# Optimization experiments

Hardware: AMD Instinct MI355X
Metric: run time of the kernel (lower is better)

Reference implementation:

```python
import jax, jax.numpy as jnp
import numpy as np

B, SEQ, DIM = 2, 2048, 1024
H = 16
DH = DIM // H            # 64, head dim; LayerNorm is over this axis
LAT = 512
CTX = SEQ - LAT          # 1536
SCALE = DH ** -0.5
LN_EPS = 1e-5


def _rotary_cos_sin(n):
    # lucidrains RotaryEmbedding: inv_freq = 1/10000^(2i/d); emb = cat(freqs, freqs)
    inv_freq = 1.0 / (10000.0 ** (jnp.arange(0, DH, 2, dtype=jnp.float32) / DH))
    freqs = jnp.arange(n, dtype=jnp.float32)[:, None] * inv_freq[None, :]
    emb = jnp.concatenate([freqs, freqs], axis=-1)  # [n, DH]
    return jnp.cos(emb), jnp.sin(emb)


def _rotate_half(t):
    t1, t2 = jnp.split(t, 2, axis=-1)
    return jnp.concatenate([-t2, t1], axis=-1)


def _layernorm(t, g, b):
    m = jnp.mean(t, axis=-1, keepdims=True)
    v = jnp.var(t, axis=-1, keepdims=True)
    return (t - m) / jnp.sqrt(v + LN_EPS) * g + b


def setup_inputs() -> dict:
    key = jax.random.key(0)
    ks = jax.random.split(key, 4)
    x = jax.random.normal(ks[0], (B, SEQ, DIM), dtype=jnp.float32)
    Wq = jax.random.normal(ks[1], (DIM, DIM), dtype=jnp.float32) * 0.02
    Wkv = jax.random.normal(ks[2], (DIM, DIM), dtype=jnp.float32) * 0.02
    Wo = jax.random.normal(ks[3], (DIM, DIM), dtype=jnp.float32) * 0.02
    bo = jnp.zeros((DIM,), dtype=jnp.float32)
    ln_g = jnp.ones((DH,), dtype=jnp.float32)
    ln_b = jnp.zeros((DH,), dtype=jnp.float32)
    return {"x": x, "Wq": Wq, "Wkv": Wkv, "Wo": Wo, "bo": bo, "ln_g": ln_g, "ln_b": ln_b}


def reference(x, Wq, Wkv, Wo, bo, ln_g, ln_b):
    b, n, d = x.shape
    neg = -jnp.finfo(x.dtype).max

    # projections (torch Linear: y = x @ W.T)
    q = x @ Wq.T
    kv = x @ Wkv.T

    def split_heads(t):  # b n (h d) -> (b h) n d
        return t.reshape(b, n, H, DH).transpose(0, 2, 1, 3).reshape(b * H, n, DH)

    q = split_heads(q)
    kv = split_heads(kv)

    cos, sin = _rotary_cos_sin(n)  # [n, DH], broadcasts over (b h)
    q = q * cos + _rotate_half(q) * sin
    kv = kv * cos + _rotate_half(kv) * sin

    q_lat = q[:, CTX:] * SCALE   # [(bh), LAT, DH]
    q_ctx = q[:, :CTX] * SCALE   # [(bh), CTX, DH]

    lkv = _layernorm(kv, ln_g, ln_b)       # key layernorm over head dim
    lkv_ctx = lkv[:, :CTX]                 # per-position LN => slice equals norm(kv_ctx)

    # latent branch: latent queries over full sequence, causal only on latent block
    lsim = jnp.einsum('bid,bjd->bij', q_lat, lkv)  # [(bh), LAT, n]
    lat = n - CTX
    causal = jnp.triu(jnp.ones((lat, lat), dtype=bool), 1)
    mask = jnp.concatenate([jnp.zeros((lat, CTX), dtype=bool), causal], axis=-1)
    lsim = jnp.where(mask, neg, lsim)
    attn = jax.nn.softmax(lsim, axis=-1)
    out = jnp.einsum('bij,bjd->bid', attn, lkv)    # [(bh), LAT, DH]

    # context branch: context queries over context keys, NO causal mask
    lsim_ctx = jnp.einsum('bid,bjd->bij', q_ctx, lkv_ctx)
    attn_ctx = jax.nn.softmax(lsim_ctx, axis=-1)
    out_ctx = jnp.einsum('bij,bjd->bid', attn_ctx, lkv_ctx)  # [(bh), CTX, DH]

    def merge_heads(t):  # (b h) m d -> b m (h d)
        m = t.shape[1]
        return t.reshape(b, H, m, DH).transpose(0, 2, 1, 3).reshape(b, m, H * DH)

    # original concatenates latent output FIRST, then context
    out_all = jnp.concatenate([merge_heads(out), merge_heads(out_ctx)], axis=1)
    return out_all @ Wo.T + bo
```

## Files before the change

### kernel.cpp

```cpp
#include <hip/hip_runtime.h>
#include <cstdint>
#include <cstddef>

typedef unsigned short u16;
typedef __bf16 bf16x8 __attribute__((ext_vector_type(8)));
typedef __bf16 bf16x2 __attribute__((ext_vector_type(2)));
typedef float f32x4 __attribute__((ext_vector_type(4)));
typedef float f32x16 __attribute__((ext_vector_type(16)));

#define DEV __device__ __forceinline__

DEV float bf2f(u16 v) { union { unsigned u; float f; } x; x.u = ((unsigned)v) << 16; return x.f; }
DEV u16 f2bf(float f) {
  union { float f; unsigned u; } x; x.f = f;
  unsigned u = x.u + 0x7fffu + ((x.u >> 16) & 1u);
  return (u16)(u >> 16);
}

DEV float fexp2(float x) {
#if __has_builtin(__builtin_amdgcn_exp2f)
  return __builtin_amdgcn_exp2f(x);
#else
  return exp2f(x);
#endif
}

DEV f32x4 mfma16(bf16x8 a, bf16x8 b, f32x4 c) {
  return __builtin_amdgcn_mfma_f32_16x16x32_bf16(a, b, c, 0, 0, 0);
}
DEV f32x16 mfma32(bf16x8 a, bf16x8 b, f32x16 c) {
  return __builtin_amdgcn_mfma_f32_32x32x16_bf16(a, b, c, 0, 0, 0);
}

DEV void stage16(const void* g, void* l) {
#if __has_builtin(__builtin_amdgcn_global_load_lds)
  __builtin_amdgcn_global_load_lds((__attribute__((address_space(1))) void*)g,
                                   (__attribute__((address_space(3))) void*)l, 16, 0, 0);
#else
  *(uint4*)l = *(const uint4*)g;
#endif
}

DEV unsigned pkbf(float a, float b) {
  bf16x2 v = {(__bf16)a, (__bf16)b};
  return __builtin_bit_cast(unsigned, v);
}

DEV void plswap(unsigned& a, unsigned& b) {
#if __has_builtin(__builtin_amdgcn_permlane32_swap)
  auto r = __builtin_amdgcn_permlane32_swap(a, b, false, false);
  a = (unsigned)r[0];
  b = (unsigned)r[1];
#else
  unsigned sa = __shfl_xor((int)a, 32), sb = __shfl_xor((int)b, 32);
  bool hi = ((threadIdx.x & 63) >> 5) != 0;
  unsigned na = hi ? sb : a;
  unsigned nb = hi ? b : sa;
  a = na; b = nb;
#endif
}

__global__ __launch_bounds__(256) void cvt_all(const float* __restrict__ x,
                                               const float* __restrict__ Wq,
                                               const float* __restrict__ Wkv,
                                               const float* __restrict__ Wo,
                                               u16* __restrict__ xb,
                                               u16* __restrict__ wqkv,
                                               u16* __restrict__ wo,
                                               float2* __restrict__ tab) {
  const int blk = blockIdx.x;
  if (blk >= 7168) {
    const int idx = (blk - 7168) * 256 + threadIdx.x;
    const int pos = idx >> 5, fi = idx & 31;
    float ang = (float)pos * exp2f((float)fi * -0.415241011860919f);
    float sn, cs;
    sincosf(ang, &sn, &cs);
    tab[idx] = make_float2(cs, sn);
    return;
  }
  const float* src; u16* dst; int base;
  if (blk < 4096)      { src = x;   dst = xb;             base = blk; }
  else if (blk < 5120) { src = Wq;  dst = wqkv;           base = blk - 4096; }
  else if (blk < 6144) { src = Wkv; dst = wqkv + 1048576; base = blk - 5120; }
  else                 { src = Wo;  dst = wo;             base = blk - 6144; }
  const int i = (base * 256 + threadIdx.x) * 4;
  float4 v = *(const float4*)(src + i);
  ushort4 o;
  o.x = f2bf(v.x); o.y = f2bf(v.y); o.z = f2bf(v.z); o.w = f2bf(v.w);
  *(ushort4*)(dst + i) = o;
}

__global__ __launch_bounds__(256) void gemm_qkv(const u16* __restrict__ A,
                                                const u16* __restrict__ Bm,
                                                const float2* __restrict__ tab,
                                                const float* __restrict__ lng,
                                                const float* __restrict__ lnb,
                                                u16* __restrict__ q_b,
                                                u16* __restrict__ k_b,
                                                u16* __restrict__ vT_b) {
  __shared__ u16 As[2][8192];
  __shared__ u16 Bs[2][8192];
  const int tid = threadIdx.x;
  const int lane = tid & 63;
  const int lo = lane & 15, hi = lane >> 4;
  const int wid = tid >> 6;
  const int wr = wid >> 1, wc = wid & 1;
  int lin = blockIdx.y * 16 + blockIdx.x;
  lin = (lin & 7) * 64 + (lin >> 3);
  const long m0 = (long)(lin >> 4) * 128;
  const long n0 = (long)(lin & 15) * 128;

  f32x4 acc[4][4];
  const f32x4 vzero = {0.f, 0.f, 0.f, 0.f};
#pragma unroll
  for (int i = 0; i < 4; ++i)
#pragma unroll
    for (int j = 0; j < 4; ++j) acc[i][j] = vzero;

  const char* Abase = (const char*)(A + m0 * 1024);
  const char* Bbase = (const char*)(Bm + n0 * 1024);

#pragma unroll
  for (int i = 0; i < 4; ++i) {
    int o = (i * 256 + tid) * 16;
    int row = o >> 7, kb = o & 127;
    stage16(Abase + (long)row * 2048 + kb, (char*)As[0] + o);
    stage16(Bbase + (long)row * 2048 + kb, (char*)Bs[0] + o);
  }
  __syncthreads();

  int cur = 0;
  for (int kt = 0; kt < 16; ++kt) {
    if (kt + 1 < 16) {
      const int kb0 = (kt + 1) * 128;
#pragma unroll
      for (int i = 0; i < 4; ++i) {
        int o = (i * 256 + tid) * 16;
        int row = o >> 7, kb = o & 127;
        stage16(Abase + (long)row * 2048 + kb0 + kb, (char*)As[cur ^ 1] + o);
        stage16(Bbase + (long)row * 2048 + kb0 + kb, (char*)Bs[cur ^ 1] + o);
      }
    }
#pragma unroll
    for (int ks = 0; ks < 2; ++ks) {
      bf16x8 af[4], bfr[4];
#pragma unroll
      for (int mi = 0; mi < 4; ++mi)
        af[mi] = *(const bf16x8*)&As[cur][(wr * 64 + mi * 16 + lo) * 64 + ks * 32 + hi * 8];
#pragma unroll
      for (int ni = 0; ni < 4; ++ni)
        bfr[ni] = *(const bf16x8*)&Bs[cur][(wc * 64 + ni * 16 + lo) * 64 + ks * 32 + hi * 8];
#pragma unroll
      for (int mi = 0; mi < 4; ++mi)
#pragma unroll
        for (int ni = 0; ni < 4; ++ni)
          acc[mi][ni] = mfma16(af[mi], bfr[ni], acc[mi][ni]);
    }
    __syncthreads();
    cur ^= 1;
  }

  const int brow = (int)(m0 >> 11);
  const bool isQ = (n0 < 1024);
  const int hbase = isQ ? (int)(n0 >> 6) : (int)((n0 - 1024) >> 6);
  const int h = hbase + wc;
  const int bh = brow * 16 + h;
  float lg[4], lb[4];
  if (!isQ) {
#pragma unroll
    for (int ni = 0; ni < 4; ++ni) {
      lg[ni] = lng[ni * 16 + lo];
      lb[ni] = lnb[ni * 16 + lo];
    }
  }
#pragma unroll
  for (int mi = 0; mi < 4; ++mi) {
    const int pos0 = ((int)m0 & 2047) + wr * 64 + mi * 16 + hi * 4;
    float cs[2][4], sn[2][4];
#pragma unroll
    for (int p = 0; p < 2; ++p)
#pragma unroll
      for (int r = 0; r < 4; ++r) {
        float2 t = tab[(pos0 + r) * 32 + p * 16 + lo];
        cs[p][r] = t.x; sn[p][r] = t.y;
      }
    float o[4][4];
#pragma unroll
    for (int ni = 0; ni < 4; ++ni) {
      const float sgn = (ni < 2) ? -1.f : 1.f;
#pragma unroll
      for (int r = 0; r < 4; ++r)
        o[ni][r] = acc[mi][ni][r] * cs[ni & 1][r] + sgn * acc[mi][ni ^ 2][r] * sn[ni & 1][r];
    }
    if (isQ) {
#pragma unroll
      for (int ni = 0; ni < 4; ++ni)
#pragma unroll
        for (int r = 0; r < 4; ++r)
          q_b[((size_t)bh * 2048 + pos0 + r) * 64 + ni * 16 + lo] =
              f2bf(o[ni][r] * 0.18033688f);
    } else {
      float s1[4], s2[4];
#pragma unroll
      for (int r = 0; r < 4; ++r) {
        s1[r] = o[0][r] + o[1][r] + o[2][r] + o[3][r];
        s2[r] = o[0][r] * o[0][r] + o[1][r] * o[1][r] + o[2][r] * o[2][r] + o[3][r] * o[3][r];
      }
#pragma unroll
      for (int msk = 1; msk < 16; msk <<= 1)
#pragma unroll
        for (int r = 0; r < 4; ++r) {
          s1[r] += __shfl_xor(s1[r], msk);
          s2[r] += __shfl_xor(s2[r], msk);
        }
      u16 kv16[4][4];
#pragma unroll
      for (int r = 0; r < 4; ++r) {
        const float mean = s1[r] * (1.f / 64.f);
        const float var = s2[r] * (1.f / 64.f) - mean * mean;
        const float rstd = rsqrtf(var + 1e-5f);
#pragma unroll
        for (int ni = 0; ni < 4; ++ni) {
          const float lk = (o[ni][r] - mean) * rstd * lg[ni] + lb[ni];
          kv16[ni][r] = f2bf(lk);
          k_b[((size_t)bh * 2048 + pos0 + r) * 64 + ni * 16 + lo] = kv16[ni][r];
        }
      }
#pragma unroll
      for (int ni = 0; ni < 4; ++ni) {
        ushort4 w4 = {kv16[ni][0], kv16[ni][1], kv16[ni][2], kv16[ni][3]};
        *(ushort4*)&vT_b[((size_t)bh * 64 + ni * 16 + lo) * 2048 + pos0] = w4;
      }
    }
  }
}

__global__ __launch_bounds__(256) void gemm_out(const u16* __restrict__ A,
                                                const u16* __restrict__ Bm,
                                                float* __restrict__ Cf,
                                                const float* __restrict__ bias) {
  __shared__ u16 As[2][8192];
  __shared__ u16 Bs[2][4096];
  const int tid = threadIdx.x;
  const int lane = tid & 63;
  const int lo = lane & 15, hi = lane >> 4;
  const int wid = tid >> 6;
  const int wr = wid >> 1, wc = wid & 1;
  int lin = blockIdx.y * 16 + blockIdx.x;
  lin = (lin & 7) * 64 + (lin >> 3);
  const long m0 = (long)(lin >> 4) * 128;
  const long n0 = (long)(lin & 15) * 64;

  f32x4 acc[4][2];
  const f32x4 vzero = {0.f, 0.f, 0.f, 0.f};
#pragma unroll
  for (int i = 0; i < 4; ++i) {
    acc[i][0] = vzero; acc[i][1] = vzero;
  }

  const char* Abase = (const char*)(A + m0 * 1024);
  const char* Bbase = (const char*)(Bm + n0 * 1024);

#pragma unroll
  for (int i = 0; i < 4; ++i) {
    int o = (i * 256 + tid) * 16;
    int row = o >> 7, kb = o & 127;
    stage16(Abase + (long)row * 2048 + kb, (char*)As[0] + o);
  }
#pragma unroll
  for (int i = 0; i < 2; ++i) {
    int o = (i * 256 + tid) * 16;
    int row = o >> 7, kb = o & 127;
    stage16(Bbase + (long)row * 2048 + kb, (char*)Bs[0] + o);
  }
  __syncthreads();

  int cur = 0;
  for (int kt = 0; kt < 16; ++kt) {
    if (kt + 1 < 16) {
      const int kb0 = (kt + 1) * 128;
#pragma unroll
      for (int i = 0; i < 4; ++i) {
        int o = (i * 256 + tid) * 16;
        int row = o >> 7, kb = o & 127;
        stage16(Abase + (long)row * 2048 + kb0 + kb, (char*)As[cur ^ 1] + o);
      }
#pragma unroll
      for (int i = 0; i < 2; ++i) {
        int o = (i * 256 + tid) * 16;
        int row = o >> 7, kb = o & 127;
        stage16(Bbase + (long)row * 2048 + kb0 + kb, (char*)Bs[cur ^ 1] + o);
      }
    }
#pragma unroll
    for (int ks = 0; ks < 2; ++ks) {
      bf16x8 af[4], bfr[2];
#pragma unroll
      for (int mi = 0; mi < 4; ++mi)
        af[mi] = *(const bf16x8*)&As[cur][(wr * 64 + mi * 16 + lo) * 64 + ks * 32 + hi * 8];
#pragma unroll
      for (int ni = 0; ni < 2; ++ni)
        bfr[ni] = *(const bf16x8*)&Bs[cur][(wc * 32 + ni * 16 + lo) * 64 + ks * 32 + hi * 8];
#pragma unroll
      for (int mi = 0; mi < 4; ++mi)
#pragma unroll
        for (int ni = 0; ni < 2; ++ni)
          acc[mi][ni] = mfma16(af[mi], bfr[ni], acc[mi][ni]);
    }
    __syncthreads();
    cur ^= 1;
  }
#pragma unroll
  for (int mi = 0; mi < 4; ++mi)
#pragma unroll
    for (int ni = 0; ni < 2; ++ni) {
      const long col = n0 + wc * 32 + ni * 16 + lo;
      const float bs = bias[col];
#pragma unroll
      for (int r = 0; r < 4; ++r) {
        const long row = m0 + wr * 64 + mi * 16 + hi * 4 + r;
        Cf[row * 1024 + col] = acc[mi][ni][r] + bs;
      }
    }
}

__global__ __launch_bounds__(256, 2) void attn_kernel(const u16* __restrict__ q_b,
                                                      const u16* __restrict__ k_b,
                                                      const u16* __restrict__ vT_b,
                                                      u16* __restrict__ out_all) {
  __shared__ __align__(16) char smem[65536];
  __shared__ float ldsLs[2][2][32];
  __shared__ float ldsLi[2][2][32];
  const int tid = threadIdx.x;
  const int wid = tid >> 6, lane = tid & 63;
  const int l31 = lane & 31, lh = lane >> 5;
  const int half = wid >> 1, wp = wid & 1;
  const int bid = blockIdx.x;
  const int xcd = bid & 7, rest = bid >> 3;
  const int bh = (xcd << 2) | (rest & 3);
  const int unit = rest >> 2;
  const int b = bh >> 4, h = bh & 15;
  const bool lat = unit >= 12;
  const int q0b = lat ? 1536 + (unit - 12) * 128 : unit * 128;
  const int q0w = q0b + wp * 64;
  const int nkt_tot = lat ? ((q0b + 128) >> 6) : 24;
  const int nhalf = nkt_tot >> 1;
  const int kt0 = half * nhalf;
  const int wave_kmax = lat ? (q0w + 63) : 1535;
  const char* kg = (const char*)(k_b + (size_t)bh * 2048 * 64);
  const char* vg = (const char*)(vT_b + (size_t)bh * 64 * 2048);
  char* Kbuf0 = smem + half * 32768;
  char* Kbuf1 = Kbuf0 + 8192;
  char* Vbuf0 = Kbuf0 + 16384;
  char* Vbuf1 = Kbuf0 + 24576;
  const f32x16 vzero16 = {0.f,0.f,0.f,0.f,0.f,0.f,0.f,0.f,0.f,0.f,0.f,0.f,0.f,0.f,0.f,0.f};

  bf16x8 qf[2][4];
#pragma unroll
  for (int s = 0; s < 2; ++s) {
    const u16* qrow = q_b + ((size_t)bh * 2048 + q0w + s * 32 + l31) * 64;
#pragma unroll
    for (int ds = 0; ds < 4; ++ds)
      qf[s][ds] = *(const bf16x8*)(qrow + ds * 16 + lh * 8);
  }

  float lsum[2] = {0.f, 0.f};
  f32x16 oacc[2][2];
  oacc[0][0] = vzero16; oacc[0][1] = vzero16;
  oacc[1][0] = vzero16; oacc[1][1] = vzero16;

  const int t127 = tid & 127;

  {
    const int kb0 = kt0 << 6;
#pragma unroll
    for (int i = 0; i < 4; ++i) {
      const int off = t127 * 16 + i * 2048;
      const int row = off >> 7, colb = off & 127;
      const int sc = colb ^ ((row & 7) << 4);
      stage16(kg + (size_t)(kb0 + row) * 128 + sc, Kbuf0 + off);
      stage16(vg + (size_t)row * 4096 + (size_t)(kb0 << 1) + sc, Vbuf0 + off);
    }
  }

  for (int t = 0; t < nhalf; ++t) {
    const int kt = kt0 + t;
    const int k0 = kt << 6;
    const bool more = (t + 1 < nhalf);
    const char* Kc = (t & 1) ? Kbuf1 : Kbuf0;
    const char* Vc = (t & 1) ? Vbuf1 : Vbuf0;
    char* Kn = (t & 1) ? Kbuf0 : Kbuf1;
    char* Vn = (t & 1) ? Vbuf0 : Vbuf1;
    if (more) {
      const int k0n = k0 + 64;
#pragma unroll
      for (int i = 0; i < 4; ++i) {
        const int off = t127 * 16 + i * 2048;
        const int row = off >> 7, colb = off & 127;
        const int sc = colb ^ ((row & 7) << 4);
        stage16(kg + (size_t)(k0n + row) * 128 + sc, Kn + off);
        stage16(vg + (size_t)row * 4096 + (size_t)(k0n << 1) + sc, Vn + off);
      }
      asm volatile("s_waitcnt vmcnt(8)" ::: "memory");
    } else {
      asm volatile("s_waitcnt vmcnt(0)" ::: "memory");
    }
    __builtin_amdgcn_s_barrier();
    __builtin_amdgcn_sched_barrier(0);
    if (k0 <= wave_kmax) {
      const int sw = (l31 & 7) << 4;
      bf16x8 kfr[2][4];
      bf16x8 bv[4][2];
#pragma unroll
      for (int kb = 0; kb < 2; ++kb) {
        const char* kr = Kc + (kb * 32 + l31) * 128;
#pragma unroll
        for (int ds = 0; ds < 4; ++ds)
          kfr[kb][ds] = *(const bf16x8*)(kr + ((ds * 32 + lh * 16) ^ sw));
      }
#pragma unroll
      for (int db = 0; db < 2; ++db) {
        const char* vr = Vc + (db * 32 + l31) * 128;
#pragma unroll
        for (int t4 = 0; t4 < 4; ++t4)
          bv[t4][db] = *(const bf16x8*)(vr + ((t4 * 32 + lh * 16) ^ sw));
      }
      f32x16 s32[2][2];
      __builtin_amdgcn_s_setprio(1);
#pragma unroll
      for (int kb = 0; kb < 2; ++kb)
#pragma unroll
        for (int s = 0; s < 2; ++s) {
          f32x16 acc = vzero16;
#pragma unroll
          for (int ds = 0; ds < 4; ++ds)
            acc = mfma32(kfr[kb][ds], qf[s][ds], acc);
          s32[s][kb] = acc;
        }
      __builtin_amdgcn_s_setprio(0);
      unsigned w[2][16];
#pragma unroll
      for (int s = 0; s < 2; ++s) {
        if (lat && (k0 + 63 > q0w + s * 32)) {
          const int qg = q0w + s * 32 + l31;
#pragma unroll
          for (int kb = 0; kb < 2; ++kb)
#pragma unroll
            for (int r = 0; r < 16; ++r) {
              const int key = k0 + kb * 32 + (r & 3) + 8 * (r >> 2) + 4 * lh;
              if (key > qg) s32[s][kb][r] = -1e30f;
            }
        }
#pragma unroll
        for (int kb = 0; kb < 2; ++kb) {
          float p[16];
#pragma unroll
          for (int r = 0; r < 16; ++r) {
            p[r] = fexp2(s32[s][kb][r]);
            lsum[s] += p[r];
          }
#pragma unroll
          for (int m = 0; m < 8; ++m) w[s][kb * 8 + m] = pkbf(p[2 * m], p[2 * m + 1]);
        }
      }
#pragma unroll
      for (int t4 = 0; t4 < 4; ++t4) {
        const int g = t4 * 4;
        union { unsigned uw[4]; bf16x8 v; } A[2];
#pragma unroll
        for (int s = 0; s < 2; ++s) {
          plswap(w[s][g], w[s][g + 2]);
          plswap(w[s][g + 1], w[s][g + 3]);
          A[s].uw[0] = w[s][g];     A[s].uw[1] = w[s][g + 1];
          A[s].uw[2] = w[s][g + 2]; A[s].uw[3] = w[s][g + 3];
        }
        __builtin_amdgcn_s_setprio(1);
#pragma unroll
        for (int db = 0; db < 2; ++db) {
          oacc[0][db] = mfma32(A[0].v, bv[t4][db], oacc[0][db]);
          oacc[1][db] = mfma32(A[1].v, bv[t4][db], oacc[1][db]);
        }
        __builtin_amdgcn_s_setprio(0);
      }
    }
    __builtin_amdgcn_sched_barrier(0);
    __builtin_amdgcn_s_barrier();
  }

  float* mergeO = (float*)smem + (size_t)wp * 4096;
  if (half == 1) {
#pragma unroll
    for (int s = 0; s < 2; ++s) {
      float ls = lsum[s] + __shfl_xor(lsum[s], 32);
      if (lh == 0) ldsLs[wp][s][l31] = ls;
#pragma unroll
      for (int db = 0; db < 2; ++db)
#pragma unroll
        for (int r = 0; r < 16; ++r) {
          const int qv = (r & 3) + 8 * (r >> 2) + 4 * lh;
          mergeO[(s * 32 + qv) * 64 + db * 32 + l31] = oacc[s][db][r];
        }
    }
  }
  __syncthreads();
  if (half == 0) {
#pragma unroll
    for (int s = 0; s < 2; ++s) {
      float ls = lsum[s] + __shfl_xor(lsum[s], 32) + ldsLs[wp][s][l31];
      if (lh == 0) ldsLi[wp][s][l31] = 1.f / ls;
    }
    const int orow0 = lat ? (q0w - 1536) : (512 + q0w);
#pragma unroll
    for (int s = 0; s < 2; ++s)
#pragma unroll
      for (int db = 0; db < 2; ++db)
#pragma unroll
        for (int r = 0; r < 16; ++r) {
          const int qv = (r & 3) + 8 * (r >> 2) + 4 * lh;
          const float o = oacc[s][db][r] + mergeO[(s * 32 + qv) * 64 + db * 32 + l31];
          out_all[((size_t)b * 2048 + orow0 + s * 32 + qv) * 1024 + h * 64 + db * 32 + l31] =
              f2bf(o * ldsLi[wp][s][qv]);
        }
  }
}

extern "C" void kernel_launch(void* const* d_in, const int* in_sizes, int n_in,
                              void* d_out, int out_size, void* d_ws, size_t ws_size,
                              hipStream_t stream) {
  const float* x    = (const float*)d_in[0];
  const float* Wq   = (const float*)d_in[1];
  const float* Wkv  = (const float*)d_in[2];
  const float* Wo   = (const float*)d_in[3];
  const float* bo   = (const float*)d_in[4];
  const float* ln_g = (const float*)d_in[5];
  const float* ln_b = (const float*)d_in[6];
  float* out = (float*)d_out;
  char* ws = (char*)d_ws;

  u16*    xb      = (u16*)(ws + 0);
  u16*    out_all = (u16*)(ws + 0);
  u16*    wqkv_b  = (u16*)(ws + (size_t)(8u << 20));
  u16*    wo_b    = (u16*)(ws + (size_t)(12u << 20));
  float2* tab     = (float2*)(ws + (size_t)(14u << 20));
  u16*    q_b     = (u16*)(ws + (size_t)(15u << 20));
  u16*    k_b     = (u16*)(ws + (size_t)(23u << 20));
  u16*    vT_b    = (u16*)(ws + (size_t)(31u << 20));

  cvt_all<<<7424, 256, 0, stream>>>(x, Wq, Wkv, Wo, xb, wqkv_b, wo_b, tab);
  gemm_qkv<<<dim3(16, 32), 256, 0, stream>>>(xb, wqkv_b, tab, ln_g, ln_b,
                                             q_b, k_b, vT_b);
  attn_kernel<<<512, 256, 0, stream>>>(q_b, k_b, vT_b, out_all);
  gemm_out<<<dim3(16, 32), 256, 0, stream>>>(out_all, wo_b, out, bo);
}
```

Before: 114.8 us.

## Pipeline GEMM loads with partial vmcnt waits and square XCD tile mapping

Both projection GEMMs now issue the next k-tile's async global-to-LDS loads and then wait only for the previous tile (partial vmcnt), using raw s_barrier plus sched_barrier in place of full __syncthreads. This lets the prefetch overlap the MFMA work of the current tile instead of draining every load at each barrier. Block indices are also remapped so that each XCD gets a square 8x8 region of tiles, which is meant to improve L2 reuse of A and B panels. The hand-counted vmcnt values depend on how many loads the compiler emits per stage, so a wrong count could create a race.

```diff
diff --git a/kernel.cpp b/kernel.cpp
--- a/kernel.cpp
+++ b/kernel.cpp
@@ -58,6 +58,12 @@
   unsigned nb = hi ? b : sa;
   a = na; b = nb;
 #endif
+}
+
+DEV void xcd_square(int lin, int& mt, int& nt) {
+  const int x = lin & 7, i = lin >> 3;
+  mt = ((x & 3) << 3) | (i >> 3);
+  nt = ((x >> 2) << 3) | (i & 7);
 }
 
 __global__ __launch_bounds__(256) void cvt_all(const float* __restrict__ x,
@@ -105,10 +111,10 @@
   const int lo = lane & 15, hi = lane >> 4;
   const int wid = tid >> 6;
   const int wr = wid >> 1, wc = wid & 1;
-  int lin = blockIdx.y * 16 + blockIdx.x;
-  lin = (lin & 7) * 64 + (lin >> 3);
-  const long m0 = (long)(lin >> 4) * 128;
-  const long n0 = (long)(lin & 15) * 128;
+  int mt, nt;
+  xcd_square(blockIdx.y * 16 + blockIdx.x, mt, nt);
+  const long m0 = (long)mt * 128;
+  const long n0 = (long)nt * 128;
 
   f32x4 acc[4][4];
   const f32x4 vzero = {0.f, 0.f, 0.f, 0.f};
@@ -127,7 +133,6 @@
     stage16(Abase + (long)row * 2048 + kb, (char*)As[0] + o);
     stage16(Bbase + (long)row * 2048 + kb, (char*)Bs[0] + o);
   }
-  __syncthreads();
 
   int cur = 0;
   for (int kt = 0; kt < 16; ++kt) {
@@ -140,7 +145,12 @@
         stage16(Abase + (long)row * 2048 + kb0 + kb, (char*)As[cur ^ 1] + o);
         stage16(Bbase + (long)row * 2048 + kb0 + kb, (char*)Bs[cur ^ 1] + o);
       }
-    }
+      asm volatile("s_waitcnt vmcnt(8)" ::: "memory");
+    } else {
+      asm volatile("s_waitcnt vmcnt(0)" ::: "memory");
+    }
+    __builtin_amdgcn_s_barrier();
+    __builtin_amdgcn_sched_barrier(0);
 #pragma unroll
     for (int ks = 0; ks < 2; ++ks) {
       bf16x8 af[4], bfr[4];
@@ -156,7 +166,8 @@
         for (int ni = 0; ni < 4; ++ni)
           acc[mi][ni] = mfma16(af[mi], bfr[ni], acc[mi][ni]);
     }
-    __syncthreads();
+    __builtin_amdgcn_sched_barrier(0);
+    __builtin_amdgcn_s_barrier();
     cur ^= 1;
   }
 
@@ -246,10 +257,10 @@
   const int lo = lane & 15, hi = lane >> 4;
   const int wid = tid >> 6;
   const int wr = wid >> 1, wc = wid & 1;
-  int lin = blockIdx.y * 16 + blockIdx.x;
-  lin = (lin & 7) * 64 + (lin >> 3);
-  const long m0 = (long)(lin >> 4) * 128;
-  const long n0 = (long)(lin & 15) * 64;
+  int mt, nt;
+  xcd_square(blockIdx.y * 16 + blockIdx.x, mt, nt);
+  const long m0 = (long)mt * 128;
+  const long n0 = (long)nt * 64;
 
   f32x4 acc[4][2];
   const f32x4 vzero = {0.f, 0.f, 0.f, 0.f};
@@ -273,7 +284,6 @@
     int row = o >> 7, kb = o & 127;
     stage16(Bbase + (long)row * 2048 + kb, (char*)Bs[0] + o);
   }
-  __syncthreads();
 
   int cur = 0;
   for (int kt = 0; kt < 16; ++kt) {
@@ -291,7 +301,12 @@
         int row = o >> 7, kb = o & 127;
         stage16(Bbase + (long)row * 2048 + kb0 + kb, (char*)Bs[cur ^ 1] + o);
       }
-    }
+      asm volatile("s_waitcnt vmcnt(6)" ::: "memory");
+    } else {
+      asm volatile("s_waitcnt vmcnt(0)" ::: "memory");
+    }
+    __builtin_amdgcn_s_barrier();
+    __builtin_amdgcn_sched_barrier(0);
 #pragma unroll
     for (int ks = 0; ks < 2; ++ks) {
       bf16x8 af[4], bfr[2];
@@ -307,7 +322,8 @@
         for (int ni = 0; ni < 2; ++ni)
           acc[mi][ni] = mfma16(af[mi], bfr[ni], acc[mi][ni]);
     }
-    __syncthreads();
+    __builtin_amdgcn_sched_barrier(0);
+    __builtin_amdgcn_s_barrier();
     cur ^= 1;
   }
 #pragma unroll
```

Measured after the change: 110.8 us. 1.04x faster.
